# Optimization experiments

Hardware: AMD Instinct MI355X
Metric: run time of the kernel (lower is better)

The kernel has to match this reference:

```python
import jax, jax.numpy as jnp
import numpy as np

B, N, C = 8, 4096, 256
HEADS, SR = 8, 4
LN_EPS = 1e-5

def setup_inputs() -> dict:
    key = jax.random.key(0)
    ks = jax.random.split(key, 8)
    std = 0.02
    x = jax.random.normal(ks[0], (B, N, C), dtype=jnp.float32)
    q_w = jax.random.normal(ks[1], (C, C), dtype=jnp.float32) * std          # [in,out]
    kv_w = jax.random.normal(ks[2], (C, 2 * C), dtype=jnp.float32) * std     # [in,2*out]
    fan_out = SR * SR * C
    sr_w = jax.random.normal(ks[3], (C, C, SR, SR), dtype=jnp.float32) * np.sqrt(2.0 / fan_out)  # OIHW
    sr_b = jnp.zeros((C,), dtype=jnp.float32)
    ln_w = jnp.ones((C,), dtype=jnp.float32)
    ln_b = jnp.zeros((C,), dtype=jnp.float32)
    proj_w = jax.random.normal(ks[4], (C, C), dtype=jnp.float32) * std
    proj_b = jnp.zeros((C,), dtype=jnp.float32)
    return {"x": x, "H": 64, "W": 64, "q_w": q_w, "kv_w": kv_w, "sr_w": sr_w,
            "sr_b": sr_b, "ln_w": ln_w, "ln_b": ln_b, "proj_w": proj_w, "proj_b": proj_b}


def reference(x, H, W, q_w, kv_w, sr_w, sr_b, ln_w, ln_b, proj_w, proj_b):
    Bb, Nn, Cc = x.shape
    hd = Cc // HEADS
    scale = hd ** -0.5
    # q: [B, heads, N, hd]
    q = (x @ q_w).reshape(Bb, Nn, HEADS, hd).transpose(0, 2, 1, 3)
    # spatial reduction: conv(stride=sr) + LayerNorm
    x_ = x.transpose(0, 2, 1).reshape(Bb, Cc, H, W)
    x_ = jax.lax.conv_general_dilated(
        x_, sr_w, window_strides=(SR, SR), padding="VALID",
        dimension_numbers=("NCHW", "OIHW", "NCHW")) + sr_b[None, :, None, None]
    x_ = x_.reshape(Bb, Cc, -1).transpose(0, 2, 1)  # [B, Nk, C]
    mu = x_.mean(-1, keepdims=True)
    var = x_.var(-1, keepdims=True)
    x_ = (x_ - mu) * jax.lax.rsqrt(var + LN_EPS) * ln_w + ln_b
    # kv: [B, Nk, 2, heads, hd]
    Nk = x_.shape[1]
    kv = (x_ @ kv_w).reshape(Bb, Nk, 2, HEADS, hd)
    k = kv[:, :, 0].transpose(0, 2, 1, 3)  # [B, heads, Nk, hd]
    v = kv[:, :, 1].transpose(0, 2, 1, 3)  # [B, heads, Nk, hd]
    attn = jnp.einsum("bhnd,bhmd->bhnm", q, k) * scale
    attn = jax.nn.softmax(attn, axis=-1)
    out = jnp.einsum("bhnm,bhmd->bhnd", attn, v)  # [B, heads, N, hd]
    out = out.transpose(0, 2, 1, 3).reshape(Bb, Nn, Cc)
    return out @ proj_w + proj_b
```

## Files before the change

### kernel.cpp

```cpp
#include <hip/hip_runtime.h>
#include <hip/hip_bf16.h>
#include <math.h>

#define DI __device__ __forceinline__

static constexpr float SCALE = 0.17677669529663687f;

typedef short bf16x8 __attribute__((ext_vector_type(8)));
typedef float f32x4 __attribute__((ext_vector_type(4)));

__device__ unsigned short g_qw2[(size_t)256 * 8 * 64];
__device__ unsigned short g_kvw2[(size_t)512 * 8 * 64];
__device__ unsigned short g_pw2[(size_t)256 * 8 * 64];
__device__ unsigned short g_wt2[(size_t)256 * 128 * 64];
__device__ unsigned short g_x2[(size_t)32768 * 8 * 64];
__device__ unsigned short g_ln2[(size_t)2048 * 8 * 64];
__device__ unsigned short g_q[(size_t)64 * 4096 * 32];
__device__ unsigned short g_k[(size_t)64 * 256 * 32];
__device__ unsigned short g_vt[(size_t)64 * 32 * 256];
__device__ unsigned short g_convp[(size_t)16 * 2048 * 256];
__device__ unsigned short g_attnb[(size_t)32768 * 256];

DI float bfbits2f(unsigned short b) { return __uint_as_float(((unsigned)b) << 16); }

DI unsigned short f2bf(float f) {
  unsigned u = __float_as_uint(f);
  unsigned r = (u + 0x7fffu + ((u >> 16) & 1u)) >> 16;
  return (unsigned short)r;
}

DI float4 ld_bf4(const unsigned short* p) {
  ushort4 u = *(const ushort4*)p;
  return make_float4(bfbits2f(u.x), bfbits2f(u.y), bfbits2f(u.z), bfbits2f(u.w));
}

DI float ld1(const void* p, size_t i, int f32) {
  return f32 ? ((const float*)p)[i] : bfbits2f(((const unsigned short*)p)[i]);
}

DI float4 ld4(const void* p, size_t i, int f32) {
  if (f32) return *(const float4*)((const float*)p + i);
  return ld_bf4((const unsigned short*)p + i);
}

typedef const __attribute__((address_space(1))) void* gas_p;
typedef __attribute__((address_space(3))) void* las_p;
DI void gload16(const unsigned short* g, short* l) {
  __builtin_amdgcn_global_load_lds((gas_p)g, (las_p)l, 16, 0, 0);
}

template <int N> DI void wait_vmcnt() {
  if constexpr (N == 10) asm volatile("s_waitcnt vmcnt(10)" ::: "memory");
  else if constexpr (N == 9) asm volatile("s_waitcnt vmcnt(9)" ::: "memory");
  else asm volatile("s_waitcnt vmcnt(0)" ::: "memory");
}

DI int detect_f32(const void* xp) {
  const unsigned* p = (const unsigned*)xp;
  unsigned m0 = 0, m1 = 0;
#pragma unroll
  for (int i = 0; i < 32; ++i) {
    unsigned w = p[i];
    unsigned lo = w & 0x7fffu, hi = (w >> 16) & 0x7fffu;
    m0 = lo > m0 ? lo : m0;
    m1 = hi > m1 ? hi : m1;
  }
  unsigned mm = m0 > m1 ? m0 : m1;
  return mm >= 0x4680u ? 1 : 0;
}

__global__ void k_prep(const void* __restrict__ qw, const void* __restrict__ kvw,
                       const void* __restrict__ pwp, const void* __restrict__ srw,
                       const void* __restrict__ xp) {
  const int f32 = detect_f32(xp);
  int tidg = blockIdx.x * 256 + threadIdx.x;
  float v[8];
  unsigned short* dst;
  if (tidg < 8192) {
    int o = tidg >> 5, w = tidg & 31, k = w * 8;
#pragma unroll
    for (int j = 0; j < 8; ++j) v[j] = ld1(qw, (size_t)(k + j) * 256 + o, f32) * SCALE;
    dst = g_qw2 + ((size_t)o * 8 + (w >> 2)) * 64 + (w & 3) * 8;
  } else if (tidg < 24576) {
    int t = tidg - 8192;
    int o = t >> 5, w = t & 31, k = w * 8;
#pragma unroll
    for (int j = 0; j < 8; ++j) v[j] = ld1(kvw, (size_t)(k + j) * 512 + o, f32);
    dst = g_kvw2 + ((size_t)o * 8 + (w >> 2)) * 64 + (w & 3) * 8;
  } else if (tidg < 32768) {
    int t = tidg - 24576;
    int o = t >> 5, w = t & 31, k = w * 8;
#pragma unroll
    for (int j = 0; j < 8; ++j) v[j] = ld1(pwp, (size_t)(k + j) * 256 + o, f32);
    dst = g_pw2 + ((size_t)o * 8 + (w >> 2)) * 64 + (w & 3) * 8;
  } else if (tidg < 163840) {
    int t = tidg - 32768;
    int o = t >> 9, w = t & 511, k = w * 8;
#pragma unroll
    for (int j = 0; j < 8; ++j) {
      int kk = k + j, tap = kk >> 8, ci = kk & 255;
      v[j] = ld1(srw, (size_t)o * 4096 + (size_t)ci * 16 + tap, f32);
    }
    dst = g_wt2 + ((size_t)o * 128 + (w >> 2)) * 64 + (w & 3) * 8;
  } else {
    int t = tidg - 163840;
    int m = t >> 5, w = t & 31, k = w * 8;
    size_t base = (size_t)m * 256 + k;
    float4 a = ld4(xp, base, f32);
    float4 b = ld4(xp, base + 4, f32);
    v[0] = a.x; v[1] = a.y; v[2] = a.z; v[3] = a.w;
    v[4] = b.x; v[5] = b.y; v[6] = b.z; v[7] = b.w;
    dst = g_x2 + ((size_t)m * 8 + (w >> 2)) * 64 + (w & 3) * 8;
  }
  ushort4 h0, h1, l0, l1;
  h0.x = f2bf(v[0]); l0.x = f2bf(v[0] - bfbits2f(h0.x));
  h0.y = f2bf(v[1]); l0.y = f2bf(v[1] - bfbits2f(h0.y));
  h0.z = f2bf(v[2]); l0.z = f2bf(v[2] - bfbits2f(h0.z));
  h0.w = f2bf(v[3]); l0.w = f2bf(v[3] - bfbits2f(h0.w));
  h1.x = f2bf(v[4]); l1.x = f2bf(v[4] - bfbits2f(h1.x));
  h1.y = f2bf(v[5]); l1.y = f2bf(v[5] - bfbits2f(h1.y));
  h1.z = f2bf(v[6]); l1.z = f2bf(v[6] - bfbits2f(h1.z));
  h1.w = f2bf(v[7]); l1.w = f2bf(v[7] - bfbits2f(h1.w));
  *(ushort4*)dst        = h0;
  *(ushort4*)(dst + 4)  = h1;
  *(ushort4*)(dst + 32) = l0;
  *(ushort4*)(dst + 36) = l1;
}

template <int MODE>
DI void mgemm_body(short* smem, int bx, int nblk, int z,
                   const void* __restrict__ biasp, void* __restrict__ outp, int f32) {
  constexpr bool AH = (MODE != 3);
  constexpr int ASZ = AH ? 4096 : 2048;
  constexpr int BUF = ASZ + 16384;
  constexpr int NLD = AH ? 10 : 9;

  const int tid = threadIdx.x;
  const int m0 = bx * 64;
  const int wave = tid >> 6, lane = tid & 63;
  const int quad = lane >> 4, l15 = lane & 15;

  const int srow = tid >> 3;
  const int slot = (tid & 7) ^ (srow & 7);

  size_t abase0 = 0, abase1 = 0;
  if constexpr (MODE == 0 || MODE == 2) {
    abase0 = ((size_t)(m0 + srow) * 8) * 64 + slot * 8;
    abase1 = ((size_t)(m0 + 32 + srow) * 8) * 64 + slot * 8;
  } else if constexpr (MODE == 1) {
    const int kh = z >> 2, kw = z & 3;
#pragma unroll
    for (int r = 0; r < 2; ++r) {
      int m = m0 + r * 32 + srow;
      int bb = m >> 8, sp = m & 255;
      int oh = sp >> 4, ow = sp & 15;
      int n = (4 * oh + kh) * 64 + 4 * ow + kw;
      size_t ab = ((size_t)(bb * 4096 + n) * 8) * 64 + slot * 8;
      if (r == 0) abase0 = ab; else abase1 = ab;
    }
  } else {
    int ar = tid >> 2;
    int s3 = (tid & 3) ^ (ar & 3);
    abase0 = (size_t)(m0 + ar) * 256 + s3 * 8;
  }

  const unsigned short* Asrc =
      (MODE == 0 || MODE == 1) ? g_x2 : (MODE == 2) ? g_ln2 : g_attnb;
  const unsigned short* Bsrc = (MODE == 0) ? g_qw2 : (MODE == 1) ? g_wt2
                             : (MODE == 2) ? g_kvw2 : g_pw2;
  constexpr int NKT = (MODE == 1) ? 128 : 8;
  const size_t bbase =
      ((size_t)(nblk * 256 + srow) * NKT + (MODE == 1 ? z * 8 : 0)) * 64 + slot * 8;

  int aoff[4], boff[4];
#pragma unroll
  for (int mt = 0; mt < 4; ++mt) {
    int ar = mt * 16 + l15;
    if constexpr (AH) aoff[mt] = ar * 64 + ((quad ^ (ar & 7)) << 3);
    else              aoff[mt] = ar * 32 + ((quad ^ (ar & 3)) << 3);
  }
#pragma unroll
  for (int j = 0; j < 4; ++j) {
    int br = (4 * wave + j) * 16 + l15;
    boff[j] = br * 64 + ((quad ^ (br & 7)) << 3);
  }

  auto STAGE = [&](int it, int b) {
    short* sa = smem + b * BUF;
    short* sb = sa + ASZ;
    if constexpr (AH) {
      gload16(Asrc + abase0 + (size_t)it * 64, sa + tid * 8);
      gload16(Asrc + abase1 + (size_t)it * 64, sa + 2048 + tid * 8);
    } else {
      gload16(Asrc + abase0 + (size_t)it * 32, sa + tid * 8);
    }
#pragma unroll
    for (int r = 0; r < 8; ++r)
      gload16(Bsrc + bbase + (size_t)r * (32 * NKT * 64) + (size_t)it * 64,
              sb + tid * 8 + r * 2048);
  };

  f32x4 acc[4][4] = {};

  auto COMPUTE = [&](int cur) {
    const short* sa = smem + cur * BUF;
    const short* sb = sa + ASZ;
#pragma unroll
    for (int mt = 0; mt < 4; ++mt) {
      bf16x8 a_h = *(const bf16x8*)&sa[aoff[mt]];
      bf16x8 a_l;
      if constexpr (AH) a_l = *(const bf16x8*)&sa[aoff[mt] ^ 32];
#pragma unroll
      for (int j = 0; j < 4; ++j) {
        bf16x8 b_h = *(const bf16x8*)&sb[boff[j]];
        bf16x8 b_l = *(const bf16x8*)&sb[boff[j] ^ 32];
        f32x4 c = acc[mt][j];
        c = __builtin_amdgcn_mfma_f32_16x16x32_bf16(a_h, b_h, c, 0, 0, 0);
        if constexpr (AH)
          c = __builtin_amdgcn_mfma_f32_16x16x32_bf16(a_l, b_h, c, 0, 0, 0);
        c = __builtin_amdgcn_mfma_f32_16x16x32_bf16(a_h, b_l, c, 0, 0, 0);
        acc[mt][j] = c;
      }
    }
  };

  STAGE(0, 0);
#pragma unroll 1
  for (int it = 0; it < 7; ++it) {
    const int cur = it & 1;
    STAGE(it + 1, cur ^ 1);
    wait_vmcnt<NLD>();
    __builtin_amdgcn_s_barrier();
    __builtin_amdgcn_sched_barrier(0);
    COMPUTE(cur);
    asm volatile("" ::: "memory");
    __builtin_amdgcn_s_barrier();
    __builtin_amdgcn_sched_barrier(0);
  }
  wait_vmcnt<0>();
  __builtin_amdgcn_s_barrier();
  __builtin_amdgcn_sched_barrier(0);
  COMPUTE(1);

  const int f32o = f32;
#pragma unroll
  for (int mt = 0; mt < 4; ++mt) {
#pragma unroll
    for (int j = 0; j < 4; ++j) {
#pragma unroll
      for (int r = 0; r < 4; ++r) {
        int m = m0 + mt * 16 + quad * 4 + r;
        int c = nblk * 256 + (4 * wave + j) * 16 + l15;
        float v = acc[mt][j][r];
        if constexpr (MODE == 0) {
          int b = m >> 12, n = m & 4095;
          int h = c >> 5, d = c & 31;
          g_q[(((size_t)(b * 8 + h) * 4096 + n) << 5) + d] = f2bf(v);
        } else if constexpr (MODE == 1) {
          g_convp[((size_t)z * 2048 + m) * 256 + c] = f2bf(v);
        } else if constexpr (MODE == 2) {
          int s = c >> 8, h = (c >> 5) & 7, d = c & 31;
          int bb = m >> 8, nk = m & 255;
          if (s == 0)
            g_k[(((size_t)(bb * 8 + h) * 256 + nk) << 5) + d] = f2bf(v);
          else
            g_vt[(((size_t)(bb * 8 + h) * 32 + d) << 8) + nk] = f2bf(v);
        } else {
          float rr = v + ld1(biasp, c, f32o);
          if (f32o) ((float*)outp)[(size_t)m * 256 + c] = rr;
          else      ((unsigned short*)outp)[(size_t)m * 256 + c] = f2bf(rr);
        }
      }
    }
  }
}

__launch_bounds__(256, 2)
__global__ void k_mgemm01() {
  __shared__ __align__(16) short smem[2 * 20480];
  int bid = blockIdx.x;
  if (bid < 512) {
    mgemm_body<0>(smem, bid, 0, 0, nullptr, nullptr, 0);
  } else {
    int b2 = bid - 512;
    mgemm_body<1>(smem, b2 & 31, 0, b2 >> 5, nullptr, nullptr, 0);
  }
}

__launch_bounds__(256, 2)
__global__ void k_mgemm2() {
  __shared__ __align__(16) short smem[2 * 20480];
  mgemm_body<2>(smem, blockIdx.x, blockIdx.y, 0, nullptr, nullptr, 0);
}

__launch_bounds__(256, 2)
__global__ void k_mgemm3(const void* __restrict__ xp, const void* __restrict__ pb,
                         void* __restrict__ outp) {
  __shared__ __align__(16) short smem[2 * 18432];
  mgemm_body<3>(smem, blockIdx.x, 0, 0, pb, outp, detect_f32(xp));
}

__global__ void k_redln(const void* __restrict__ xp, const void* __restrict__ srb,
                        const void* __restrict__ lw, const void* __restrict__ lb) {
  const int f32 = detect_f32(xp);
  const int t = threadIdx.x;
  const int row = blockIdx.x * 8 + (t >> 5);
  const int l32 = t & 31;
  const int ch0 = l32 * 8;
  const size_t idx = (size_t)row * 256 + ch0;

  float c[8] = {};
#pragma unroll
  for (int zz = 0; zz < 16; ++zz) {
    uint4 u = *(const uint4*)&g_convp[(size_t)zz * (2048 * 256) + idx];
    c[0] += __uint_as_float(u.x << 16); c[1] += __uint_as_float(u.x & 0xffff0000u);
    c[2] += __uint_as_float(u.y << 16); c[3] += __uint_as_float(u.y & 0xffff0000u);
    c[4] += __uint_as_float(u.z << 16); c[5] += __uint_as_float(u.z & 0xffff0000u);
    c[6] += __uint_as_float(u.w << 16); c[7] += __uint_as_float(u.w & 0xffff0000u);
  }
  float4 b0 = ld4(srb, ch0, f32), b1 = ld4(srb, ch0 + 4, f32);
  c[0] += b0.x; c[1] += b0.y; c[2] += b0.z; c[3] += b0.w;
  c[4] += b1.x; c[5] += b1.y; c[6] += b1.z; c[7] += b1.w;

  float s = 0.f, sq = 0.f;
#pragma unroll
  for (int j = 0; j < 8; ++j) { s += c[j]; sq += c[j] * c[j]; }
#pragma unroll
  for (int off = 16; off >= 1; off >>= 1) {
    s += __shfl_xor(s, off, 32);
    sq += __shfl_xor(sq, off, 32);
  }
  float mu = s * (1.0f / 256.0f);
  float var = sq * (1.0f / 256.0f) - mu * mu;
  float rr = rsqrtf(var + 1e-5f);

  float4 w0 = ld4(lw, ch0, f32), w1 = ld4(lw, ch0 + 4, f32);
  float4 e0 = ld4(lb, ch0, f32), e1 = ld4(lb, ch0 + 4, f32);
  float wv[8] = {w0.x, w0.y, w0.z, w0.w, w1.x, w1.y, w1.z, w1.w};
  float ev[8] = {e0.x, e0.y, e0.z, e0.w, e1.x, e1.y, e1.z, e1.w};

  float o[8];
#pragma unroll
  for (int j = 0; j < 8; ++j) o[j] = (c[j] - mu) * rr * wv[j] + ev[j];

  ushort4 h0, h1, l0, l1;
  h0.x = f2bf(o[0]); l0.x = f2bf(o[0] - bfbits2f(h0.x));
  h0.y = f2bf(o[1]); l0.y = f2bf(o[1] - bfbits2f(h0.y));
  h0.z = f2bf(o[2]); l0.z = f2bf(o[2] - bfbits2f(h0.z));
  h0.w = f2bf(o[3]); l0.w = f2bf(o[3] - bfbits2f(h0.w));
  h1.x = f2bf(o[4]); l1.x = f2bf(o[4] - bfbits2f(h1.x));
  h1.y = f2bf(o[5]); l1.y = f2bf(o[5] - bfbits2f(h1.y));
  h1.z = f2bf(o[6]); l1.z = f2bf(o[6] - bfbits2f(h1.z));
  h1.w = f2bf(o[7]); l1.w = f2bf(o[7] - bfbits2f(h1.w));

  const size_t dbase = ((size_t)row * 8 + (l32 >> 2)) * 64 + (l32 & 3) * 8;
  *(ushort4*)&g_ln2[dbase]          = h0;
  *(ushort4*)&g_ln2[dbase + 4]      = h1;
  *(ushort4*)&g_ln2[dbase + 32]     = l0;
  *(ushort4*)&g_ln2[dbase + 36]     = l1;
}

__launch_bounds__(256, 4)
__global__ void k_attn() {
  __shared__ short smem[18688];
  short* sk  = smem;
  short* svt = smem + 10240;

  const int tid = threadIdx.x;
  const int bh = blockIdx.y;
  const int b = bh >> 3, h = bh & 7;

  {
    const uint4* gk = (const uint4*)(g_k + (size_t)bh * 8192);
    const uint4* gv = (const uint4*)(g_vt + (size_t)bh * 8192);
    for (int i = tid; i < 1024; i += 256) {
      int key = i >> 2, part = i & 3;
      *(uint4*)&sk[key * 40 + part * 8] = gk[i];
      int d = i >> 5, off = (i & 31) * 8;
      *(uint4*)&svt[d * 264 + off] = gv[i];
    }
  }
  __syncthreads();

  const int wave = tid >> 6, lane = tid & 63;
  const int quad = lane >> 4, l15 = lane & 15;
  const int n0 = blockIdx.x * 64 + wave * 16;

  bf16x8 qv = *(const bf16x8*)(g_q + ((size_t)bh * 4096 + n0 + l15) * 32 + quad * 8);

  f32x4 sacc[16];
#pragma unroll
  for (int t = 0; t < 16; ++t) {
    bf16x8 kf = *(const bf16x8*)&sk[(t * 16 + l15) * 40 + quad * 8];
    f32x4 c = {0.f, 0.f, 0.f, 0.f};
    sacc[t] = __builtin_amdgcn_mfma_f32_16x16x32_bf16(kf, qv, c, 0, 0, 0);
  }

  float m = sacc[0][0];
#pragma unroll
  for (int t = 0; t < 16; ++t) {
#pragma unroll
    for (int r = 0; r < 4; ++r) m = fmaxf(m, sacc[t][r]);
  }
  m = fmaxf(m, __shfl_xor(m, 16, 64));
  m = fmaxf(m, __shfl_xor(m, 32, 64));

  unsigned plo[16], phi[16];
  float ls = 0.f;
#pragma unroll
  for (int t = 0; t < 16; ++t) {
    unsigned short p0 = f2bf(__expf(sacc[t][0] - m));
    unsigned short p1 = f2bf(__expf(sacc[t][1] - m));
    unsigned short p2 = f2bf(__expf(sacc[t][2] - m));
    unsigned short p3 = f2bf(__expf(sacc[t][3] - m));
    ls += bfbits2f(p0) + bfbits2f(p1) + bfbits2f(p2) + bfbits2f(p3);
    plo[t] = (unsigned)p0 | ((unsigned)p1 << 16);
    phi[t] = (unsigned)p2 | ((unsigned)p3 << 16);
  }
  ls += __shfl_xor(ls, 16, 64);
  ls += __shfl_xor(ls, 32, 64);
  float inv = 1.0f / ls;

  f32x4 o0 = {0.f, 0.f, 0.f, 0.f}, o1 = {0.f, 0.f, 0.f, 0.f};
  const int laneA = ((quad & 1) << 5) + l15;
  const int laneB = laneA + 16;
  const bool hiT = quad >= 2;
#pragma unroll
  for (int c = 0; c < 8; ++c) {
    unsigned a0 = __shfl(plo[2 * c], laneA, 64), b0 = __shfl(plo[2 * c + 1], laneA, 64);
    unsigned a1 = __shfl(phi[2 * c], laneA, 64), b1 = __shfl(phi[2 * c + 1], laneA, 64);
    unsigned a2 = __shfl(plo[2 * c], laneB, 64), b2 = __shfl(plo[2 * c + 1], laneB, 64);
    unsigned a3 = __shfl(phi[2 * c], laneB, 64), b3 = __shfl(phi[2 * c + 1], laneB, 64);
    uint4 pk = make_uint4(hiT ? b0 : a0, hiT ? b1 : a1, hiT ? b2 : a2, hiT ? b3 : a3);
    bf16x8 pf = *(bf16x8*)&pk;
    bf16x8 v0 = *(const bf16x8*)&svt[l15 * 264 + c * 32 + quad * 8];
    bf16x8 v1 = *(const bf16x8*)&svt[(16 + l15) * 264 + c * 32 + quad * 8];
    o0 = __builtin_amdgcn_mfma_f32_16x16x32_bf16(v0, pf, o0, 0, 0, 0);
    o1 = __builtin_amdgcn_mfma_f32_16x16x32_bf16(v1, pf, o1, 0, 0, 0);
  }

  size_t base = ((size_t)(b * 4096 + n0 + l15)) * 256 + h * 32 + quad * 4;
  ushort4 u0, u1;
  u0.x = f2bf(o0[0] * inv); u0.y = f2bf(o0[1] * inv);
  u0.z = f2bf(o0[2] * inv); u0.w = f2bf(o0[3] * inv);
  u1.x = f2bf(o1[0] * inv); u1.y = f2bf(o1[1] * inv);
  u1.z = f2bf(o1[2] * inv); u1.w = f2bf(o1[3] * inv);
  *(ushort4*)&g_attnb[base]      = u0;
  *(ushort4*)&g_attnb[base + 16] = u1;
}

extern "C" void kernel_launch(void* const* d_in, const int* in_sizes, int n_in,
                              void* d_out, int out_size, void* d_ws, size_t ws_size,
                              hipStream_t stream) {
  const void* x   = d_in[0];
  const void* qw  = d_in[3];
  const void* kvw = d_in[4];
  const void* srw = d_in[5];
  const void* srb = d_in[6];
  const void* lnw = d_in[7];
  const void* lnb = d_in[8];
  const void* pw  = d_in[9];
  const void* pb  = d_in[10];

  k_prep<<<4736, 256, 0, stream>>>(qw, kvw, pw, srw, x);
  k_mgemm01<<<1024, 256, 0, stream>>>();
  k_redln<<<256, 256, 0, stream>>>(x, srb, lnw, lnb);
  k_mgemm2<<<dim3(32, 2), 256, 0, stream>>>();
  k_attn<<<dim3(64, 64), 256, 0, stream>>>();
  k_mgemm3<<<512, 256, 0, stream>>>(x, pb, d_out);
}
```

Measured before the change: 219.3 us.

## Halve GEMM N-tile to 128 and split conv K into 4 chunks

The shared GEMM body now uses a 64x128 output tile instead of 64x256. That halves the B staging buffer and accumulators, raising occupancy hints and doubling the grid along N for all GEMM kernels. The conv GEMM now splits K over 4 kernel rows of 32 tiles each instead of 16 positions of 8 tiles, so k_redln sums 4 partials instead of 16. The cost is more A-tile reloads across N blocks and longer per-block conv loops.

```diff
diff --git a/kernel.cpp b/kernel.cpp
--- a/kernel.cpp
+++ b/kernel.cpp
@@ -50,8 +50,8 @@
 }
 
 template <int N> DI void wait_vmcnt() {
-  if constexpr (N == 10) asm volatile("s_waitcnt vmcnt(10)" ::: "memory");
-  else if constexpr (N == 9) asm volatile("s_waitcnt vmcnt(9)" ::: "memory");
+  if constexpr (N == 6) asm volatile("s_waitcnt vmcnt(6)" ::: "memory");
+  else if constexpr (N == 5) asm volatile("s_waitcnt vmcnt(5)" ::: "memory");
   else asm volatile("s_waitcnt vmcnt(0)" ::: "memory");
 }
 
@@ -132,8 +132,10 @@
                    const void* __restrict__ biasp, void* __restrict__ outp, int f32) {
   constexpr bool AH = (MODE != 3);
   constexpr int ASZ = AH ? 4096 : 2048;
-  constexpr int BUF = ASZ + 16384;
-  constexpr int NLD = AH ? 10 : 9;
+  constexpr int BUF = ASZ + 8192;
+  constexpr int NLD = AH ? 6 : 5;
+  constexpr int NIT = (MODE == 1) ? 32 : 8;
+  constexpr int NKT = (MODE == 1) ? 128 : 8;
 
   const int tid = threadIdx.x;
   const int m0 = bx * 64;
@@ -143,36 +145,32 @@
   const int srow = tid >> 3;
   const int slot = (tid & 7) ^ (srow & 7);
 
-  size_t abase0 = 0, abase1 = 0;
+  size_t arow0 = 0, arow1 = 0, abase3 = 0;
   if constexpr (MODE == 0 || MODE == 2) {
-    abase0 = ((size_t)(m0 + srow) * 8) * 64 + slot * 8;
-    abase1 = ((size_t)(m0 + 32 + srow) * 8) * 64 + slot * 8;
+    arow0 = m0 + srow;
+    arow1 = m0 + 32 + srow;
   } else if constexpr (MODE == 1) {
-    const int kh = z >> 2, kw = z & 3;
 #pragma unroll
     for (int r = 0; r < 2; ++r) {
       int m = m0 + r * 32 + srow;
       int bb = m >> 8, sp = m & 255;
       int oh = sp >> 4, ow = sp & 15;
-      int n = (4 * oh + kh) * 64 + 4 * ow + kw;
-      size_t ab = ((size_t)(bb * 4096 + n) * 8) * 64 + slot * 8;
-      if (r == 0) abase0 = ab; else abase1 = ab;
+      size_t rb = (size_t)bb * 4096 + (4 * oh + z) * 64 + 4 * ow;
+      if (r == 0) arow0 = rb; else arow1 = rb;
     }
   } else {
     int ar = tid >> 2;
     int s3 = (tid & 3) ^ (ar & 3);
-    abase0 = (size_t)(m0 + ar) * 256 + s3 * 8;
+    abase3 = (size_t)(m0 + ar) * 256 + s3 * 8;
   }
 
   const unsigned short* Asrc =
       (MODE == 0 || MODE == 1) ? g_x2 : (MODE == 2) ? g_ln2 : g_attnb;
   const unsigned short* Bsrc = (MODE == 0) ? g_qw2 : (MODE == 1) ? g_wt2
                              : (MODE == 2) ? g_kvw2 : g_pw2;
-  constexpr int NKT = (MODE == 1) ? 128 : 8;
-  const size_t bbase =
-      ((size_t)(nblk * 256 + srow) * NKT + (MODE == 1 ? z * 8 : 0)) * 64 + slot * 8;
-
-  int aoff[4], boff[4];
+  const int brow0 = nblk * 128 + srow;
+
+  int aoff[4], boff[2];
 #pragma unroll
   for (int mt = 0; mt < 4; ++mt) {
     int ar = mt * 16 + l15;
@@ -180,27 +178,32 @@
     else              aoff[mt] = ar * 32 + ((quad ^ (ar & 3)) << 3);
   }
 #pragma unroll
-  for (int j = 0; j < 4; ++j) {
-    int br = (4 * wave + j) * 16 + l15;
+  for (int j = 0; j < 2; ++j) {
+    int br = wave * 32 + j * 16 + l15;
     boff[j] = br * 64 + ((quad ^ (br & 7)) << 3);
   }
 
   auto STAGE = [&](int it, int b) {
     short* sa = smem + b * BUF;
     short* sb = sa + ASZ;
-    if constexpr (AH) {
-      gload16(Asrc + abase0 + (size_t)it * 64, sa + tid * 8);
-      gload16(Asrc + abase1 + (size_t)it * 64, sa + 2048 + tid * 8);
+    if constexpr (MODE == 0 || MODE == 2) {
+      gload16(Asrc + (arow0 * 8 + it) * 64 + slot * 8, sa + tid * 8);
+      gload16(Asrc + (arow1 * 8 + it) * 64 + slot * 8, sa + 2048 + tid * 8);
+    } else if constexpr (MODE == 1) {
+      const int kw = it >> 3, ktA = it & 7;
+      gload16(Asrc + ((arow0 + kw) * 8 + ktA) * 64 + slot * 8, sa + tid * 8);
+      gload16(Asrc + ((arow1 + kw) * 8 + ktA) * 64 + slot * 8, sa + 2048 + tid * 8);
     } else {
-      gload16(Asrc + abase0 + (size_t)it * 32, sa + tid * 8);
-    }
-#pragma unroll
-    for (int r = 0; r < 8; ++r)
-      gload16(Bsrc + bbase + (size_t)r * (32 * NKT * 64) + (size_t)it * 64,
+      gload16(Asrc + abase3 + (size_t)it * 32, sa + tid * 8);
+    }
+    const int ktB = (MODE == 1) ? (z * 32 + (it >> 3) * 8 + (it & 7)) : it;
+#pragma unroll
+    for (int r = 0; r < 4; ++r)
+      gload16(Bsrc + ((size_t)(brow0 + r * 32) * NKT + ktB) * 64 + slot * 8,
               sb + tid * 8 + r * 2048);
   };
 
-  f32x4 acc[4][4] = {};
+  f32x4 acc[4][2] = {};
 
   auto COMPUTE = [&](int cur) {
     const short* sa = smem + cur * BUF;
@@ -211,7 +214,7 @@
       bf16x8 a_l;
       if constexpr (AH) a_l = *(const bf16x8*)&sa[aoff[mt] ^ 32];
 #pragma unroll
-      for (int j = 0; j < 4; ++j) {
+      for (int j = 0; j < 2; ++j) {
         bf16x8 b_h = *(const bf16x8*)&sb[boff[j]];
         bf16x8 b_l = *(const bf16x8*)&sb[boff[j] ^ 32];
         f32x4 c = acc[mt][j];
@@ -226,7 +229,7 @@
 
   STAGE(0, 0);
 #pragma unroll 1
-  for (int it = 0; it < 7; ++it) {
+  for (int it = 0; it < NIT - 1; ++it) {
     const int cur = it & 1;
     STAGE(it + 1, cur ^ 1);
     wait_vmcnt<NLD>();
@@ -240,17 +243,17 @@
   wait_vmcnt<0>();
   __builtin_amdgcn_s_barrier();
   __builtin_amdgcn_sched_barrier(0);
-  COMPUTE(1);
+  COMPUTE((NIT - 1) & 1);
 
   const int f32o = f32;
 #pragma unroll
   for (int mt = 0; mt < 4; ++mt) {
 #pragma unroll
-    for (int j = 0; j < 4; ++j) {
+    for (int j = 0; j < 2; ++j) {
 #pragma unroll
       for (int r = 0; r < 4; ++r) {
         int m = m0 + mt * 16 + quad * 4 + r;
-        int c = nblk * 256 + (4 * wave + j) * 16 + l15;
+        int c = nblk * 128 + wave * 32 + j * 16 + l15;
         float v = acc[mt][j][r];
         if constexpr (MODE == 0) {
           int b = m >> 12, n = m & 4095;
@@ -275,29 +278,30 @@
   }
 }
 
-__launch_bounds__(256, 2)
+__launch_bounds__(256, 3)
 __global__ void k_mgemm01() {
-  __shared__ __align__(16) short smem[2 * 20480];
+  __shared__ __align__(16) short smem[2 * 12288];
   int bid = blockIdx.x;
-  if (bid < 512) {
-    mgemm_body<0>(smem, bid, 0, 0, nullptr, nullptr, 0);
+  if (bid < 256) {
+    int m = bid & 31, nb = (bid >> 5) & 1, z = bid >> 6;
+    mgemm_body<1>(smem, m, nb, z, nullptr, nullptr, 0);
   } else {
-    int b2 = bid - 512;
-    mgemm_body<1>(smem, b2 & 31, 0, b2 >> 5, nullptr, nullptr, 0);
-  }
-}
-
-__launch_bounds__(256, 2)
+    int b2 = bid - 256;
+    mgemm_body<0>(smem, b2 >> 1, b2 & 1, 0, nullptr, nullptr, 0);
+  }
+}
+
+__launch_bounds__(256, 3)
 __global__ void k_mgemm2() {
-  __shared__ __align__(16) short smem[2 * 20480];
+  __shared__ __align__(16) short smem[2 * 12288];
   mgemm_body<2>(smem, blockIdx.x, blockIdx.y, 0, nullptr, nullptr, 0);
 }
 
-__launch_bounds__(256, 2)
+__launch_bounds__(256, 4)
 __global__ void k_mgemm3(const void* __restrict__ xp, const void* __restrict__ pb,
                          void* __restrict__ outp) {
-  __shared__ __align__(16) short smem[2 * 18432];
-  mgemm_body<3>(smem, blockIdx.x, 0, 0, pb, outp, detect_f32(xp));
+  __shared__ __align__(16) short smem[2 * 10240];
+  mgemm_body<3>(smem, blockIdx.x, blockIdx.y, 0, pb, outp, detect_f32(xp));
 }
 
 __global__ void k_redln(const void* __restrict__ xp, const void* __restrict__ srb,
@@ -311,7 +315,7 @@
 
   float c[8] = {};
 #pragma unroll
-  for (int zz = 0; zz < 16; ++zz) {
+  for (int zz = 0; zz < 4; ++zz) {
     uint4 u = *(const uint4*)&g_convp[(size_t)zz * (2048 * 256) + idx];
     c[0] += __uint_as_float(u.x << 16); c[1] += __uint_as_float(u.x & 0xffff0000u);
     c[2] += __uint_as_float(u.y << 16); c[3] += __uint_as_float(u.y & 0xffff0000u);
@@ -463,9 +467,9 @@
   const void* pb  = d_in[10];
 
   k_prep<<<4736, 256, 0, stream>>>(qw, kvw, pw, srw, x);
-  k_mgemm01<<<1024, 256, 0, stream>>>();
+  k_mgemm01<<<1280, 256, 0, stream>>>();
   k_redln<<<256, 256, 0, stream>>>(x, srb, lnw, lnb);
-  k_mgemm2<<<dim3(32, 2), 256, 0, stream>>>();
+  k_mgemm2<<<dim3(32, 4), 256, 0, stream>>>();
   k_attn<<<dim3(64, 64), 256, 0, stream>>>();
-  k_mgemm3<<<512, 256, 0, stream>>>(x, pb, d_out);
-}
+  k_mgemm3<<<dim3(512, 2), 256, 0, stream>>>(x, pb, d_out);
+}
```

New measurement: 211.8 us. -3.4%, faster.
